# Kernel tuning notes

Measured on AMD Instinct MI355X. Metric: run time of the kernel, lower is better.

The kernel has to match this reference:

```python
import jax, jax.numpy as jnp
import numpy as np

EMBED_DIM = 768
NUM_HEADS = 12
HEAD_DIM = EMBED_DIM // NUM_HEADS


def setup_inputs() -> dict:
    key = jax.random.key(0)
    ks = jax.random.split(key, 9)
    B, S, D = 2, 2048, EMBED_DIM
    scale = 1.0 / np.sqrt(D)
    x = jax.random.normal(ks[0], (B, S, D), dtype=jnp.float32)
    Wq = jax.random.normal(ks[1], (D, D), dtype=jnp.float32) * scale
    bq = jax.random.normal(ks[2], (D,), dtype=jnp.float32) * 0.01
    Wk = jax.random.normal(ks[3], (D, D), dtype=jnp.float32) * scale
    bk = jax.random.normal(ks[4], (D,), dtype=jnp.float32) * 0.01
    Wv = jax.random.normal(ks[5], (D, D), dtype=jnp.float32) * scale
    bv = jax.random.normal(ks[6], (D,), dtype=jnp.float32) * 0.01
    Wo = jax.random.normal(ks[7], (D, D), dtype=jnp.float32) * scale
    bo = jax.random.normal(ks[8], (D,), dtype=jnp.float32) * 0.01
    return {"x": x, "Wq": Wq, "bq": bq, "Wk": Wk, "bk": bk,
            "Wv": Wv, "bv": bv, "Wo": Wo, "bo": bo}


def reference(x, Wq, bq, Wk, bk, Wv, bv, Wo, bo):
    B, S, D = x.shape
    H, Dh = NUM_HEADS, HEAD_DIM
    # separate QKV projections (weights stored [in, out] so y = x @ W + b)
    q = (x @ Wq + bq).reshape(B, S, H, Dh)
    k = (x @ Wk + bk).reshape(B, S, H, Dh)
    v = (x @ Wv + bv).reshape(B, S, H, Dh)
    # NOTE: original module applies NO 1/sqrt(head_dim) scaling
    scores = jnp.einsum('bqhd,bkhd->bhqk', q, k)          # [B,H,S,S] materialized
    attn = jax.nn.softmax(scores, axis=-1)
    ctx = jnp.einsum('bhqk,bkhd->bqhd', attn, v)          # [B,S,H,Dh]
    out = ctx.reshape(B, S, D) @ Wo + bo
    return out
```

## Files before the change

kernel.cpp:

```cpp
#include <hip/hip_runtime.h>
#include <hip/hip_bf16.h>


typedef __attribute__((ext_vector_type(8))) short short8;
typedef __attribute__((ext_vector_type(4))) float float4e;

__device__ __forceinline__ ushort f2bf(float f) {
    union { float f; unsigned u; } v; v.f = f;
    unsigned r = v.u + 0x7FFF + ((v.u >> 16) & 1);
    return (ushort)(r >> 16);
}

__global__ __launch_bounds__(256) void cast_f32_bf16(
    const float* __restrict__ in, ushort* __restrict__ out, int n4)
{
    int i = blockIdx.x * blockDim.x + threadIdx.x;
    if (i < n4) {
        float4 v = *(const float4*)&in[(size_t)i * 4];
        ushort4 o;
        o.x = f2bf(v.x); o.y = f2bf(v.y); o.z = f2bf(v.z); o.w = f2bf(v.w);
        *(ushort4*)&out[(size_t)i * 4] = o;
    }
}

__global__ __launch_bounds__(256) void transpose_cast_w(
    const float* __restrict__ W, ushort* __restrict__ Wt)
{
    __shared__ float t[64][65];
    const int tid = threadIdx.x;
    const int c  = tid & 63;
    const int rg = tid >> 6;
    const int k0 = blockIdx.y * 64, n0 = blockIdx.x * 64;
    #pragma unroll
    for (int r = 0; r < 16; ++r) {
        const int row = rg * 16 + r;
        t[row][c] = W[(size_t)(k0 + row) * 768 + n0 + c];
    }
    __syncthreads();
    #pragma unroll
    for (int r = 0; r < 16; ++r) {
        const int row = rg * 16 + r;
        Wt[(size_t)(n0 + row) * 768 + k0 + c] = f2bf(t[c][row]);
    }
}

__global__ __launch_bounds__(256) void transpose_v(
    const ushort* __restrict__ Vb, ushort* __restrict__ VT)
{
    __shared__ ushort t[64][72];
    const int tid = threadIdx.x;
    const int b = blockIdx.z, h = blockIdx.y, s0 = blockIdx.x * 64;
    const int lr = tid >> 3;
    const int lc = (tid & 7) * 8;

    #pragma unroll
    for (int half = 0; half < 64; half += 32) {
        const int row = lr + half;
        *(uint4*)&t[row][lc] =
            *(const uint4*)&Vb[(size_t)(b * 2048 + s0 + row) * 768 + h * 64 + lc];
    }
    __syncthreads();
    #pragma unroll
    for (int half = 0; half < 64; half += 32) {
        const int d = lr + half;
        ushort tmp[8];
        #pragma unroll
        for (int i = 0; i < 8; ++i) tmp[i] = t[lc + i][d];
        *(uint4*)&VT[((size_t)(b * 12 + h) * 64 + d) * 2048 + s0 + lc] =
            *(const uint4*)tmp;
    }
}

__global__ __launch_bounds__(256) void gemm_qkv_fused(
    const ushort* __restrict__ A, const ushort* __restrict__ Bt,
    const float* __restrict__ bq, const float* __restrict__ bk,
    const float* __restrict__ bv, ushort* __restrict__ Outbase)
{
    constexpr int K = 768;
    __shared__ ushort As[128][40];
    __shared__ ushort Bs[128][40];

    const int tid  = threadIdx.x;
    const int w    = tid >> 6;
    const int lane = tid & 63;
    const int l16  = lane & 15;
    const int quad = lane >> 4;
    const int wr   = (w >> 1) * 64;
    const int wc   = (w & 1) * 64;
    const int row0 = blockIdx.y * 128, col0 = blockIdx.x * 128;
    const int sr = tid >> 2, sc = (tid & 3) * 8;

    float4e acc[4][4];
    #pragma unroll
    for (int mi = 0; mi < 4; ++mi)
        #pragma unroll
        for (int ni = 0; ni < 4; ++ni) acc[mi][ni] = (float4e){0.f,0.f,0.f,0.f};

    uint4 a0 = *(const uint4*)&A [(size_t)(row0 + sr     ) * K + sc];
    uint4 a1 = *(const uint4*)&A [(size_t)(row0 + sr + 64) * K + sc];
    uint4 b0 = *(const uint4*)&Bt[(size_t)(col0 + sr     ) * K + sc];
    uint4 b1 = *(const uint4*)&Bt[(size_t)(col0 + sr + 64) * K + sc];

    for (int k0 = 0; k0 < K; k0 += 32) {
        *(uint4*)&As[sr     ][sc] = a0;
        *(uint4*)&As[sr + 64][sc] = a1;
        *(uint4*)&Bs[sr     ][sc] = b0;
        *(uint4*)&Bs[sr + 64][sc] = b1;
        __syncthreads();

        if (k0 + 32 < K) {
            const int kn = k0 + 32;
            a0 = *(const uint4*)&A [(size_t)(row0 + sr     ) * K + kn + sc];
            a1 = *(const uint4*)&A [(size_t)(row0 + sr + 64) * K + kn + sc];
            b0 = *(const uint4*)&Bt[(size_t)(col0 + sr     ) * K + kn + sc];
            b1 = *(const uint4*)&Bt[(size_t)(col0 + sr + 64) * K + kn + sc];
        }

        short8 af[4], bf[4];
        #pragma unroll
        for (int i = 0; i < 4; ++i) {
            af[i] = *(const short8*)&As[wr + i * 16 + l16][quad * 8];
            bf[i] = *(const short8*)&Bs[wc + i * 16 + l16][quad * 8];
        }
        #pragma unroll
        for (int mi = 0; mi < 4; ++mi)
            #pragma unroll
            for (int ni = 0; ni < 4; ++ni)
                acc[mi][ni] = __builtin_amdgcn_mfma_f32_16x16x32_bf16(
                    af[mi], bf[ni], acc[mi][ni], 0, 0, 0);
        __syncthreads();
    }

    const int seg = (col0 >= 1536) ? 2 : (col0 >= 768 ? 1 : 0);
    const float* bias = (seg == 0) ? bq : (seg == 1) ? bk : bv;
    const int ncol0 = col0 - seg * 768 + wc;
    ushort* outp = Outbase + (size_t)seg * (4096u * 768u);

    #pragma unroll
    for (int ni = 0; ni < 4; ++ni) {
        const int col = ncol0 + ni * 16 + l16;
        const float bs = bias[col];
        #pragma unroll
        for (int mi = 0; mi < 4; ++mi) {
            #pragma unroll
            for (int r = 0; r < 4; ++r) {
                const int row = row0 + wr + mi * 16 + quad * 4 + r;
                outp[(size_t)row * 768 + col] = f2bf(acc[mi][ni][r] + bs);
            }
        }
    }
}

__global__ __launch_bounds__(256) void gemm_bt_bias_f32(
    const ushort* __restrict__ A, const ushort* __restrict__ Bt,
    const float* __restrict__ bias, float* __restrict__ Cout,
    int M, int N, int K)
{
    __shared__ ushort As[64][40];
    __shared__ ushort Bs[64][40];

    const int tid  = threadIdx.x;
    const int w    = tid >> 6;
    const int lane = tid & 63;
    const int l16  = lane & 15;
    const int quad = lane >> 4;
    const int row0 = blockIdx.y * 64, col0 = blockIdx.x * 64;
    const int sr = tid >> 2, sc = (tid & 3) * 8;

    float4e acc[4];
    #pragma unroll
    for (int n = 0; n < 4; ++n) acc[n] = (float4e){0.f, 0.f, 0.f, 0.f};

    for (int k0 = 0; k0 < K; k0 += 32) {
        *(uint4*)&As[sr][sc] = *(const uint4*)&A [(size_t)(row0 + sr) * K + k0 + sc];
        *(uint4*)&Bs[sr][sc] = *(const uint4*)&Bt[(size_t)(col0 + sr) * K + k0 + sc];
        __syncthreads();

        const short8 a = *(const short8*)&As[w * 16 + l16][quad * 8];
        #pragma unroll
        for (int n = 0; n < 4; ++n) {
            const short8 b = *(const short8*)&Bs[n * 16 + l16][quad * 8];
            acc[n] = __builtin_amdgcn_mfma_f32_16x16x32_bf16(a, b, acc[n], 0, 0, 0);
        }
        __syncthreads();
    }

    #pragma unroll
    for (int n = 0; n < 4; ++n) {
        const int col = col0 + n * 16 + l16;
        const float bs = bias[col];
        #pragma unroll
        for (int r = 0; r < 4; ++r) {
            const int row = row0 + w * 16 + quad * 4 + r;
            Cout[(size_t)row * N + col] = acc[n][r] + bs;
        }
    }
}

__global__ __launch_bounds__(256) void attn_mfma(
    const ushort* __restrict__ Qg, const ushort* __restrict__ Kgl,
    const ushort* __restrict__ VT, ushort* __restrict__ Ctx)
{
    constexpr int S = 2048, D = 768;
    __shared__ ushort Ks [64][72];
    __shared__ ushort Vts[64][72];
    __shared__ ushort Ps [64][72];

    const int tid  = threadIdx.x;
    const int w    = tid >> 6;
    const int lane = tid & 63;
    const int l16  = lane & 15;
    const int quad = lane >> 4;
    const int b = blockIdx.z, h = blockIdx.y, q0 = blockIdx.x * 64;
    const size_t hc = (size_t)h * 64;

    const size_t qoff = (size_t)(b * S + q0 + w * 16 + l16) * D + hc + quad * 8;
    const short8 yq0 = *(const short8*)&Qg[qoff];
    const short8 yq1 = *(const short8*)&Qg[qoff + 32];

    float m_ = -1e30f, l_ = 0.f;
    float4e oa[4];
    #pragma unroll
    for (int n = 0; n < 4; ++n) oa[n] = (float4e){0.f, 0.f, 0.f, 0.f};

    const int sr = tid >> 2;
    const int sc = (tid & 3) * 16;
    const size_t vtb = ((size_t)(b * 12 + h) * 64 + sr) * 2048;

    uint4 kA, kB, vA, vB;
    {
        const size_t gk = (size_t)(b * S + sr) * D + hc + sc;
        kA = *(const uint4*)&Kgl[gk];
        kB = *(const uint4*)&Kgl[gk + 8];
        vA = *(const uint4*)&VT[vtb + sc];
        vB = *(const uint4*)&VT[vtb + sc + 8];
    }

    for (int k0 = 0; k0 < S; k0 += 64) {
        *(uint4*)&Ks [sr][sc    ] = kA;
        *(uint4*)&Ks [sr][sc + 8] = kB;
        *(uint4*)&Vts[sr][sc    ] = vA;
        *(uint4*)&Vts[sr][sc + 8] = vB;
        __syncthreads();

        if (k0 + 64 < S) {
            const size_t gk = (size_t)(b * S + k0 + 64 + sr) * D + hc + sc;
            kA = *(const uint4*)&Kgl[gk];
            kB = *(const uint4*)&Kgl[gk + 8];
            vA = *(const uint4*)&VT[vtb + k0 + 64 + sc];
            vB = *(const uint4*)&VT[vtb + k0 + 64 + sc + 8];
        }

        float4e sa[4];
        #pragma unroll
        for (int kb = 0; kb < 4; ++kb) {
            const short8 xk0 = *(const short8*)&Ks[kb * 16 + l16][quad * 8];
            const short8 xk1 = *(const short8*)&Ks[kb * 16 + l16][32 + quad * 8];
            float4e z = (float4e){0.f, 0.f, 0.f, 0.f};
            z      = __builtin_amdgcn_mfma_f32_16x16x32_bf16(xk0, yq0, z, 0, 0, 0);
            sa[kb] = __builtin_amdgcn_mfma_f32_16x16x32_bf16(xk1, yq1, z, 0, 0, 0);
        }

        float mx = -1e30f;
        #pragma unroll
        for (int kb = 0; kb < 4; ++kb)
            #pragma unroll
            for (int r = 0; r < 4; ++r) mx = fmaxf(mx, sa[kb][r]);
        mx = fmaxf(mx, __shfl_xor(mx, 16, 64));
        mx = fmaxf(mx, __shfl_xor(mx, 32, 64));
        const float mn = fmaxf(m_, mx);
        const float alpha = __expf(m_ - mn);
        float p[4][4], ps = 0.f;
        #pragma unroll
        for (int kb = 0; kb < 4; ++kb)
            #pragma unroll
            for (int r = 0; r < 4; ++r) {
                p[kb][r] = __expf(sa[kb][r] - mn);
                ps += p[kb][r];
            }
        ps += __shfl_xor(ps, 16, 64);
        ps += __shfl_xor(ps, 32, 64);
        l_ = l_ * alpha + ps;
        m_ = mn;

        #pragma unroll
        for (int kb = 0; kb < 4; ++kb) {
            ushort4 pk;
            pk.x = f2bf(p[kb][0]); pk.y = f2bf(p[kb][1]);
            pk.z = f2bf(p[kb][2]); pk.w = f2bf(p[kb][3]);
            *(ushort4*)&Ps[w * 16 + l16][kb * 16 + quad * 4] = pk;
        }

        #pragma unroll
        for (int n = 0; n < 4; ++n)
            #pragma unroll
            for (int r = 0; r < 4; ++r) oa[n][r] *= alpha;

        const short8 yp0 = *(const short8*)&Ps[w * 16 + l16][quad * 8];
        const short8 yp1 = *(const short8*)&Ps[w * 16 + l16][32 + quad * 8];
        #pragma unroll
        for (int db = 0; db < 4; ++db) {
            const short8 xv0 = *(const short8*)&Vts[db * 16 + l16][quad * 8];
            const short8 xv1 = *(const short8*)&Vts[db * 16 + l16][32 + quad * 8];
            oa[db] = __builtin_amdgcn_mfma_f32_16x16x32_bf16(xv0, yp0, oa[db], 0, 0, 0);
            oa[db] = __builtin_amdgcn_mfma_f32_16x16x32_bf16(xv1, yp1, oa[db], 0, 0, 0);
        }
        __syncthreads();
    }

    const float inv = 1.0f / l_;
    const size_t crow = (size_t)(b * S + q0 + w * 16 + l16) * D + hc;
    #pragma unroll
    for (int db = 0; db < 4; ++db) {
        ushort4 ov;
        ov.x = f2bf(oa[db][0] * inv); ov.y = f2bf(oa[db][1] * inv);
        ov.z = f2bf(oa[db][2] * inv); ov.w = f2bf(oa[db][3] * inv);
        *(ushort4*)&Ctx[crow + db * 16 + quad * 4] = ov;
    }
}

extern "C" void kernel_launch(void* const* d_in, const int* in_sizes, int n_in,
                              void* d_out, int out_size, void* d_ws, size_t ws_size,
                              hipStream_t stream)
{
    const float* x  = (const float*)d_in[0];
    const float* Wq = (const float*)d_in[1];
    const float* bq = (const float*)d_in[2];
    const float* Wk = (const float*)d_in[3];
    const float* bk = (const float*)d_in[4];
    const float* Wv = (const float*)d_in[5];
    const float* bv = (const float*)d_in[6];
    const float* Wo = (const float*)d_in[7];
    const float* bo = (const float*)d_in[8];

    const int M = 4096, D = 768;
    const size_t XE = (size_t)M * D;
    const size_t WE = (size_t)D * D;

    ushort* xb   = (ushort*)d_ws;
    ushort* wtq  = xb   + XE;
    ushort* wtk  = wtq  + WE;
    ushort* wtv  = wtk  + WE;
    ushort* wto  = wtv  + WE;
    ushort* qb   = wto  + WE;
    ushort* kb   = qb   + XE;
    ushort* vb   = kb   + XE;
    ushort* ctxb = vb   + XE;
    ushort* vt   = xb;

    cast_f32_bf16<<<(int)(XE / 4 / 256), 256, 0, stream>>>(x, xb, (int)(XE / 4));

    const dim3 gt(12, 12);
    transpose_cast_w<<<gt, 256, 0, stream>>>(Wq, wtq);
    transpose_cast_w<<<gt, 256, 0, stream>>>(Wk, wtk);
    transpose_cast_w<<<gt, 256, 0, stream>>>(Wv, wtv);
    transpose_cast_w<<<gt, 256, 0, stream>>>(Wo, wto);

    gemm_qkv_fused<<<dim3(2304 / 128, 4096 / 128), 256, 0, stream>>>(
        xb, wtq, bq, bk, bv, qb);

    transpose_v<<<dim3(32, 12, 2), 256, 0, stream>>>(vb, vt);

    attn_mfma<<<dim3(2048 / 64, 12, 2), 256, 0, stream>>>(qb, kb, vt, ctxb);

    gemm_bt_bias_f32<<<dim3(D / 64, M / 64), 256, 0, stream>>>(
        ctxb, wto, bo, (float*)d_out, M, D, D);
}
```

Baseline: 209.8 us.

## Enlarge attention KV tile, use 128x128 output GEMM, batch weight transposes

```diff
diff --git a/kernel.cpp b/kernel.cpp
--- a/kernel.cpp
+++ b/kernel.cpp
@@ -23,10 +23,16 @@
     }
 }
 
-__global__ __launch_bounds__(256) void transpose_cast_w(
-    const float* __restrict__ W, ushort* __restrict__ Wt)
+__global__ __launch_bounds__(256) void transpose_cast_w4(
+    const float* __restrict__ W0, const float* __restrict__ W1,
+    const float* __restrict__ W2, const float* __restrict__ W3,
+    ushort* __restrict__ WtBase)
 {
     __shared__ float t[64][65];
+    const int z = blockIdx.z;
+    const float* W = (z == 0) ? W0 : (z == 1) ? W1 : (z == 2) ? W2 : W3;
+    ushort* Wt = WtBase + (size_t)z * (768u * 768u);
+
     const int tid = threadIdx.x;
     const int c  = tid & 63;
     const int rg = tid >> 6;
@@ -151,48 +157,76 @@
     }
 }
 
-__global__ __launch_bounds__(256) void gemm_bt_bias_f32(
+__global__ __launch_bounds__(256) void gemm_wo_128(
     const ushort* __restrict__ A, const ushort* __restrict__ Bt,
-    const float* __restrict__ bias, float* __restrict__ Cout,
-    int M, int N, int K)
-{
-    __shared__ ushort As[64][40];
-    __shared__ ushort Bs[64][40];
+    const float* __restrict__ bias, float* __restrict__ Cout)
+{
+    constexpr int K = 768, N = 768;
+    __shared__ ushort As[128][40];
+    __shared__ ushort Bs[128][40];
 
     const int tid  = threadIdx.x;
     const int w    = tid >> 6;
     const int lane = tid & 63;
     const int l16  = lane & 15;
     const int quad = lane >> 4;
-    const int row0 = blockIdx.y * 64, col0 = blockIdx.x * 64;
+    const int wr   = (w >> 1) * 64;
+    const int wc   = (w & 1) * 64;
+    const int row0 = blockIdx.y * 128, col0 = blockIdx.x * 128;
     const int sr = tid >> 2, sc = (tid & 3) * 8;
 
-    float4e acc[4];
-    #pragma unroll
-    for (int n = 0; n < 4; ++n) acc[n] = (float4e){0.f, 0.f, 0.f, 0.f};
+    float4e acc[4][4];
+    #pragma unroll
+    for (int mi = 0; mi < 4; ++mi)
+        #pragma unroll
+        for (int ni = 0; ni < 4; ++ni) acc[mi][ni] = (float4e){0.f,0.f,0.f,0.f};
+
+    uint4 a0 = *(const uint4*)&A [(size_t)(row0 + sr     ) * K + sc];
+    uint4 a1 = *(const uint4*)&A [(size_t)(row0 + sr + 64) * K + sc];
+    uint4 b0 = *(const uint4*)&Bt[(size_t)(col0 + sr     ) * K + sc];
+    uint4 b1 = *(const uint4*)&Bt[(size_t)(col0 + sr + 64) * K + sc];
 
     for (int k0 = 0; k0 < K; k0 += 32) {
-        *(uint4*)&As[sr][sc] = *(const uint4*)&A [(size_t)(row0 + sr) * K + k0 + sc];
-        *(uint4*)&Bs[sr][sc] = *(const uint4*)&Bt[(size_t)(col0 + sr) * K + k0 + sc];
-        __syncthreads();
-
-        const short8 a = *(const short8*)&As[w * 16 + l16][quad * 8];
-        #pragma unroll
-        for (int n = 0; n < 4; ++n) {
-            const short8 b = *(const short8*)&Bs[n * 16 + l16][quad * 8];
-            acc[n] = __builtin_amdgcn_mfma_f32_16x16x32_bf16(a, b, acc[n], 0, 0, 0);
-        }
-        __syncthreads();
-    }
-
-    #pragma unroll
-    for (int n = 0; n < 4; ++n) {
-        const int col = col0 + n * 16 + l16;
+        *(uint4*)&As[sr     ][sc] = a0;
+        *(uint4*)&As[sr + 64][sc] = a1;
+        *(uint4*)&Bs[sr     ][sc] = b0;
+        *(uint4*)&Bs[sr + 64][sc] = b1;
+        __syncthreads();
+
+        if (k0 + 32 < K) {
+            const int kn = k0 + 32;
+            a0 = *(const uint4*)&A [(size_t)(row0 + sr     ) * K + kn + sc];
+            a1 = *(const uint4*)&A [(size_t)(row0 + sr + 64) * K + kn + sc];
+            b0 = *(const uint4*)&Bt[(size_t)(col0 + sr     ) * K + kn + sc];
+            b1 = *(const uint4*)&Bt[(size_t)(col0 + sr + 64) * K + kn + sc];
+        }
+
+        short8 af[4], bf[4];
+        #pragma unroll
+        for (int i = 0; i < 4; ++i) {
+            af[i] = *(const short8*)&As[wr + i * 16 + l16][quad * 8];
+            bf[i] = *(const short8*)&Bs[wc + i * 16 + l16][quad * 8];
+        }
+        #pragma unroll
+        for (int mi = 0; mi < 4; ++mi)
+            #pragma unroll
+            for (int ni = 0; ni < 4; ++ni)
+                acc[mi][ni] = __builtin_amdgcn_mfma_f32_16x16x32_bf16(
+                    af[mi], bf[ni], acc[mi][ni], 0, 0, 0);
+        __syncthreads();
+    }
+
+    #pragma unroll
+    for (int ni = 0; ni < 4; ++ni) {
+        const int col = col0 + wc + ni * 16 + l16;
         const float bs = bias[col];
         #pragma unroll
-        for (int r = 0; r < 4; ++r) {
-            const int row = row0 + w * 16 + quad * 4 + r;
-            Cout[(size_t)row * N + col] = acc[n][r] + bs;
+        for (int mi = 0; mi < 4; ++mi) {
+            #pragma unroll
+            for (int r = 0; r < 4; ++r) {
+                const int row = row0 + wr + mi * 16 + quad * 4 + r;
+                Cout[(size_t)row * N + col] = acc[mi][ni][r] + bs;
+            }
         }
     }
 }
@@ -201,10 +235,10 @@
     const ushort* __restrict__ Qg, const ushort* __restrict__ Kgl,
     const ushort* __restrict__ VT, ushort* __restrict__ Ctx)
 {
-    constexpr int S = 2048, D = 768;
-    __shared__ ushort Ks [64][72];
-    __shared__ ushort Vts[64][72];
-    __shared__ ushort Ps [64][72];
+    constexpr int S = 2048, D = 768, TK = 128;
+    __shared__ ushort Ks [128][68];
+    __shared__ ushort Vts[64][136];
+    __shared__ ushort Ps [64][136];
 
     const int tid  = threadIdx.x;
     const int w    = tid >> 6;
@@ -223,37 +257,36 @@
     #pragma unroll
     for (int n = 0; n < 4; ++n) oa[n] = (float4e){0.f, 0.f, 0.f, 0.f};
 
-    const int sr = tid >> 2;
-    const int sc = (tid & 3) * 16;
-    const size_t vtb = ((size_t)(b * 12 + h) * 64 + sr) * 2048;
-
-    uint4 kA, kB, vA, vB;
-    {
-        const size_t gk = (size_t)(b * S + sr) * D + hc + sc;
-        kA = *(const uint4*)&Kgl[gk];
-        kB = *(const uint4*)&Kgl[gk + 8];
-        vA = *(const uint4*)&VT[vtb + sc];
-        vB = *(const uint4*)&VT[vtb + sc + 8];
-    }
-
-    for (int k0 = 0; k0 < S; k0 += 64) {
-        *(uint4*)&Ks [sr][sc    ] = kA;
-        *(uint4*)&Ks [sr][sc + 8] = kB;
-        *(uint4*)&Vts[sr][sc    ] = vA;
-        *(uint4*)&Vts[sr][sc + 8] = vB;
-        __syncthreads();
-
-        if (k0 + 64 < S) {
-            const size_t gk = (size_t)(b * S + k0 + 64 + sr) * D + hc + sc;
-            kA = *(const uint4*)&Kgl[gk];
-            kB = *(const uint4*)&Kgl[gk + 8];
-            vA = *(const uint4*)&VT[vtb + k0 + 64 + sc];
-            vB = *(const uint4*)&VT[vtb + k0 + 64 + sc + 8];
-        }
-
-        float4e sa[4];
-        #pragma unroll
-        for (int kb = 0; kb < 4; ++kb) {
+    const int kr = tid >> 1, kc = (tid & 1) * 32;
+    const int dr = tid >> 2, vc = (tid & 3) * 32;
+    const size_t vtb = ((size_t)(b * 12 + h) * 64 + dr) * 2048;
+
+    uint4 kf[4], vf[4];
+    #pragma unroll
+    for (int j = 0; j < 4; ++j) {
+        kf[j] = *(const uint4*)&Kgl[(size_t)(b * S + kr) * D + hc + kc + 8 * j];
+        vf[j] = *(const uint4*)&VT[vtb + vc + 8 * j];
+    }
+
+    for (int k0 = 0; k0 < S; k0 += TK) {
+        #pragma unroll
+        for (int j = 0; j < 4; ++j) {
+            *(uint4*)&Ks [kr][kc + 8 * j] = kf[j];
+            *(uint4*)&Vts[dr][vc + 8 * j] = vf[j];
+        }
+        __syncthreads();
+
+        if (k0 + TK < S) {
+            #pragma unroll
+            for (int j = 0; j < 4; ++j) {
+                kf[j] = *(const uint4*)&Kgl[(size_t)(b * S + k0 + TK + kr) * D + hc + kc + 8 * j];
+                vf[j] = *(const uint4*)&VT[vtb + k0 + TK + vc + 8 * j];
+            }
+        }
+
+        float4e sa[8];
+        #pragma unroll
+        for (int kb = 0; kb < 8; ++kb) {
             const short8 xk0 = *(const short8*)&Ks[kb * 16 + l16][quad * 8];
             const short8 xk1 = *(const short8*)&Ks[kb * 16 + l16][32 + quad * 8];
             float4e z = (float4e){0.f, 0.f, 0.f, 0.f};
@@ -263,47 +296,43 @@
 
         float mx = -1e30f;
         #pragma unroll
-        for (int kb = 0; kb < 4; ++kb)
+        for (int kb = 0; kb < 8; ++kb)
             #pragma unroll
             for (int r = 0; r < 4; ++r) mx = fmaxf(mx, sa[kb][r]);
         mx = fmaxf(mx, __shfl_xor(mx, 16, 64));
         mx = fmaxf(mx, __shfl_xor(mx, 32, 64));
         const float mn = fmaxf(m_, mx);
         const float alpha = __expf(m_ - mn);
-        float p[4][4], ps = 0.f;
-        #pragma unroll
-        for (int kb = 0; kb < 4; ++kb)
-            #pragma unroll
-            for (int r = 0; r < 4; ++r) {
-                p[kb][r] = __expf(sa[kb][r] - mn);
-                ps += p[kb][r];
-            }
+        float ps = 0.f;
+        #pragma unroll
+        for (int kb = 0; kb < 8; ++kb) {
+            float p0 = __expf(sa[kb][0] - mn);
+            float p1 = __expf(sa[kb][1] - mn);
+            float p2 = __expf(sa[kb][2] - mn);
+            float p3 = __expf(sa[kb][3] - mn);
+            ps += (p0 + p1) + (p2 + p3);
+            ushort4 pk;
+            pk.x = f2bf(p0); pk.y = f2bf(p1); pk.z = f2bf(p2); pk.w = f2bf(p3);
+            *(ushort4*)&Ps[w * 16 + l16][kb * 16 + quad * 4] = pk;
+        }
         ps += __shfl_xor(ps, 16, 64);
         ps += __shfl_xor(ps, 32, 64);
         l_ = l_ * alpha + ps;
         m_ = mn;
 
         #pragma unroll
-        for (int kb = 0; kb < 4; ++kb) {
-            ushort4 pk;
-            pk.x = f2bf(p[kb][0]); pk.y = f2bf(p[kb][1]);
-            pk.z = f2bf(p[kb][2]); pk.w = f2bf(p[kb][3]);
-            *(ushort4*)&Ps[w * 16 + l16][kb * 16 + quad * 4] = pk;
-        }
-
-        #pragma unroll
         for (int n = 0; n < 4; ++n)
             #pragma unroll
             for (int r = 0; r < 4; ++r) oa[n][r] *= alpha;
 
-        const short8 yp0 = *(const short8*)&Ps[w * 16 + l16][quad * 8];
-        const short8 yp1 = *(const short8*)&Ps[w * 16 + l16][32 + quad * 8];
-        #pragma unroll
-        for (int db = 0; db < 4; ++db) {
-            const short8 xv0 = *(const short8*)&Vts[db * 16 + l16][quad * 8];
-            const short8 xv1 = *(const short8*)&Vts[db * 16 + l16][32 + quad * 8];
-            oa[db] = __builtin_amdgcn_mfma_f32_16x16x32_bf16(xv0, yp0, oa[db], 0, 0, 0);
-            oa[db] = __builtin_amdgcn_mfma_f32_16x16x32_bf16(xv1, yp1, oa[db], 0, 0, 0);
+        #pragma unroll
+        for (int c = 0; c < 4; ++c) {
+            const short8 yp = *(const short8*)&Ps[w * 16 + l16][c * 32 + quad * 8];
+            #pragma unroll
+            for (int db = 0; db < 4; ++db) {
+                const short8 xv = *(const short8*)&Vts[db * 16 + l16][c * 32 + quad * 8];
+                oa[db] = __builtin_amdgcn_mfma_f32_16x16x32_bf16(xv, yp, oa[db], 0, 0, 0);
+            }
         }
         __syncthreads();
     }
@@ -339,9 +368,7 @@
 
     ushort* xb   = (ushort*)d_ws;
     ushort* wtq  = xb   + XE;
-    ushort* wtk  = wtq  + WE;
-    ushort* wtv  = wtk  + WE;
-    ushort* wto  = wtv  + WE;
+    ushort* wto  = wtq  + 3 * WE;
     ushort* qb   = wto  + WE;
     ushort* kb   = qb   + XE;
     ushort* vb   = kb   + XE;
@@ -350,11 +377,7 @@
 
     cast_f32_bf16<<<(int)(XE / 4 / 256), 256, 0, stream>>>(x, xb, (int)(XE / 4));
 
-    const dim3 gt(12, 12);
-    transpose_cast_w<<<gt, 256, 0, stream>>>(Wq, wtq);
-    transpose_cast_w<<<gt, 256, 0, stream>>>(Wk, wtk);
-    transpose_cast_w<<<gt, 256, 0, stream>>>(Wv, wtv);
-    transpose_cast_w<<<gt, 256, 0, stream>>>(Wo, wto);
+    transpose_cast_w4<<<dim3(12, 12, 4), 256, 0, stream>>>(Wq, Wk, Wv, Wo, wtq);
 
     gemm_qkv_fused<<<dim3(2304 / 128, 4096 / 128), 256, 0, stream>>>(
         xb, wtq, bq, bk, bv, qb);
@@ -363,6 +386,6 @@
 
     attn_mfma<<<dim3(2048 / 64, 12, 2), 256, 0, stream>>>(qb, kb, vt, ctxb);
 
-    gemm_bt_bias_f32<<<dim3(D / 64, M / 64), 256, 0, stream>>>(
-        ctxb, wto, bo, (float*)d_out, M, D, D);
-}
+    gemm_wo_128<<<dim3(768 / 128, 4096 / 128), 256, 0, stream>>>(
+        ctxb, wto, bo, (float*)d_out);
+}
```

Result: slower. 277.8 us (+32.4%).

## Use async global-to-LDS loads in QKV GEMM, 128-tile Wo GEMM, batched weight transpose

Applied to the files above, without the earlier changes.

```diff
diff --git a/kernel.cpp b/kernel.cpp
--- a/kernel.cpp
+++ b/kernel.cpp
@@ -9,6 +9,13 @@
     union { float f; unsigned u; } v; v.f = f;
     unsigned r = v.u + 0x7FFF + ((v.u >> 16) & 1);
     return (ushort)(r >> 16);
+}
+
+__device__ __forceinline__ void async_cp16(const ushort* g, ushort* l) {
+    __builtin_amdgcn_global_load_lds(
+        (const __attribute__((address_space(1))) unsigned int*)g,
+        (__attribute__((address_space(3))) unsigned int*)l,
+        16, 0, 0);
 }
 
 __global__ __launch_bounds__(256) void cast_f32_bf16(
@@ -23,10 +30,16 @@
     }
 }
 
-__global__ __launch_bounds__(256) void transpose_cast_w(
-    const float* __restrict__ W, ushort* __restrict__ Wt)
+__global__ __launch_bounds__(256) void transpose_cast_w4(
+    const float* __restrict__ W0, const float* __restrict__ W1,
+    const float* __restrict__ W2, const float* __restrict__ W3,
+    ushort* __restrict__ WtBase)
 {
     __shared__ float t[64][65];
+    const int z = blockIdx.z;
+    const float* W = (z == 0) ? W0 : (z == 1) ? W1 : (z == 2) ? W2 : W3;
+    ushort* Wt = WtBase + (size_t)z * (768u * 768u);
+
     const int tid = threadIdx.x;
     const int c  = tid & 63;
     const int rg = tid >> 6;
@@ -77,6 +90,76 @@
     const float* __restrict__ bv, ushort* __restrict__ Outbase)
 {
     constexpr int K = 768;
+    __shared__ ushort As[128][32];
+    __shared__ ushort Bs[128][32];
+
+    const int tid  = threadIdx.x;
+    const int w    = tid >> 6;
+    const int lane = tid & 63;
+    const int l16  = lane & 15;
+    const int quad = lane >> 4;
+    const int wr   = (w >> 1) * 64;
+    const int wc   = (w & 1) * 64;
+    const int row0 = blockIdx.y * 128, col0 = blockIdx.x * 128;
+
+    const int r4 = lane >> 2;
+    const int c8 = (lane & 3) * 8;
+
+    float4e acc[4][4];
+    #pragma unroll
+    for (int mi = 0; mi < 4; ++mi)
+        #pragma unroll
+        for (int ni = 0; ni < 4; ++ni) acc[mi][ni] = (float4e){0.f,0.f,0.f,0.f};
+
+    for (int k0 = 0; k0 < K; k0 += 32) {
+        #pragma unroll
+        for (int i = 0; i < 2; ++i) {
+            const int rr = w * 32 + i * 16;
+            async_cp16(&A [(size_t)(row0 + rr + r4) * K + k0 + c8], &As[rr][0]);
+            async_cp16(&Bt[(size_t)(col0 + rr + r4) * K + k0 + c8], &Bs[rr][0]);
+        }
+        __syncthreads();
+
+        short8 af[4], bf[4];
+        #pragma unroll
+        for (int i = 0; i < 4; ++i) {
+            af[i] = *(const short8*)&As[wr + i * 16 + l16][quad * 8];
+            bf[i] = *(const short8*)&Bs[wc + i * 16 + l16][quad * 8];
+        }
+        #pragma unroll
+        for (int mi = 0; mi < 4; ++mi)
+            #pragma unroll
+            for (int ni = 0; ni < 4; ++ni)
+                acc[mi][ni] = __builtin_amdgcn_mfma_f32_16x16x32_bf16(
+                    af[mi], bf[ni], acc[mi][ni], 0, 0, 0);
+        __syncthreads();
+    }
+
+    const int seg = (col0 >= 1536) ? 2 : (col0 >= 768 ? 1 : 0);
+    const float* bias = (seg == 0) ? bq : (seg == 1) ? bk : bv;
+    const int ncol0 = col0 - seg * 768 + wc;
+    ushort* outp = Outbase + (size_t)seg * (4096u * 768u);
+
+    #pragma unroll
+    for (int ni = 0; ni < 4; ++ni) {
+        const int col = ncol0 + ni * 16 + l16;
+        const float bs = bias[col];
+        #pragma unroll
+        for (int mi = 0; mi < 4; ++mi) {
+            #pragma unroll
+            for (int r = 0; r < 4; ++r) {
+                const int row = row0 + wr + mi * 16 + quad * 4 + r;
+                outp[(size_t)row * 768 + col] = f2bf(acc[mi][ni][r] + bs);
+            }
+        }
+    }
+}
+
+__global__ __launch_bounds__(256) void gemm_wo_128(
+    const ushort* __restrict__ A, const ushort* __restrict__ Bt,
+    const float* __restrict__ bias, float* __restrict__ Cout)
+{
+    constexpr int K = 768, N = 768;
     __shared__ ushort As[128][40];
     __shared__ ushort Bs[128][40];
 
@@ -131,68 +214,17 @@
         __syncthreads();
     }
 
-    const int seg = (col0 >= 1536) ? 2 : (col0 >= 768 ? 1 : 0);
-    const float* bias = (seg == 0) ? bq : (seg == 1) ? bk : bv;
-    const int ncol0 = col0 - seg * 768 + wc;
-    ushort* outp = Outbase + (size_t)seg * (4096u * 768u);
-
     #pragma unroll
     for (int ni = 0; ni < 4; ++ni) {
-        const int col = ncol0 + ni * 16 + l16;
+        const int col = col0 + wc + ni * 16 + l16;
         const float bs = bias[col];
         #pragma unroll
         for (int mi = 0; mi < 4; ++mi) {
             #pragma unroll
             for (int r = 0; r < 4; ++r) {
                 const int row = row0 + wr + mi * 16 + quad * 4 + r;
-                outp[(size_t)row * 768 + col] = f2bf(acc[mi][ni][r] + bs);
+                Cout[(size_t)row * N + col] = acc[mi][ni][r] + bs;
             }
-        }
-    }
-}
-
-__global__ __launch_bounds__(256) void gemm_bt_bias_f32(
-    const ushort* __restrict__ A, const ushort* __restrict__ Bt,
-    const float* __restrict__ bias, float* __restrict__ Cout,
-    int M, int N, int K)
-{
-    __shared__ ushort As[64][40];
-    __shared__ ushort Bs[64][40];
-
-    const int tid  = threadIdx.x;
-    const int w    = tid >> 6;
-    const int lane = tid & 63;
-    const int l16  = lane & 15;
-    const int quad = lane >> 4;
-    const int row0 = blockIdx.y * 64, col0 = blockIdx.x * 64;
-    const int sr = tid >> 2, sc = (tid & 3) * 8;
-
-    float4e acc[4];
-    #pragma unroll
-    for (int n = 0; n < 4; ++n) acc[n] = (float4e){0.f, 0.f, 0.f, 0.f};
-
-    for (int k0 = 0; k0 < K; k0 += 32) {
-        *(uint4*)&As[sr][sc] = *(const uint4*)&A [(size_t)(row0 + sr) * K + k0 + sc];
-        *(uint4*)&Bs[sr][sc] = *(const uint4*)&Bt[(size_t)(col0 + sr) * K + k0 + sc];
-        __syncthreads();
-
-        const short8 a = *(const short8*)&As[w * 16 + l16][quad * 8];
-        #pragma unroll
-        for (int n = 0; n < 4; ++n) {
-            const short8 b = *(const short8*)&Bs[n * 16 + l16][quad * 8];
-            acc[n] = __builtin_amdgcn_mfma_f32_16x16x32_bf16(a, b, acc[n], 0, 0, 0);
-        }
-        __syncthreads();
-    }
-
-    #pragma unroll
-    for (int n = 0; n < 4; ++n) {
-        const int col = col0 + n * 16 + l16;
-        const float bs = bias[col];
-        #pragma unroll
-        for (int r = 0; r < 4; ++r) {
-            const int row = row0 + w * 16 + quad * 4 + r;
-            Cout[(size_t)row * N + col] = acc[n][r] + bs;
         }
     }
 }
@@ -339,9 +371,7 @@
 
     ushort* xb   = (ushort*)d_ws;
     ushort* wtq  = xb   + XE;
-    ushort* wtk  = wtq  + WE;
-    ushort* wtv  = wtk  + WE;
-    ushort* wto  = wtv  + WE;
+    ushort* wto  = wtq  + 3 * WE;
     ushort* qb   = wto  + WE;
     ushort* kb   = qb   + XE;
     ushort* vb   = kb   + XE;
@@ -350,11 +380,7 @@
 
     cast_f32_bf16<<<(int)(XE / 4 / 256), 256, 0, stream>>>(x, xb, (int)(XE / 4));
 
-    const dim3 gt(12, 12);
-    transpose_cast_w<<<gt, 256, 0, stream>>>(Wq, wtq);
-    transpose_cast_w<<<gt, 256, 0, stream>>>(Wk, wtk);
-    transpose_cast_w<<<gt, 256, 0, stream>>>(Wv, wtv);
-    transpose_cast_w<<<gt, 256, 0, stream>>>(Wo, wto);
+    transpose_cast_w4<<<dim3(12, 12, 4), 256, 0, stream>>>(Wq, Wk, Wv, Wo, wtq);
 
     gemm_qkv_fused<<<dim3(2304 / 128, 4096 / 128), 256, 0, stream>>>(
         xb, wtq, bq, bk, bv, qb);
@@ -363,6 +389,6 @@
 
     attn_mfma<<<dim3(2048 / 64, 12, 2), 256, 0, stream>>>(qb, kb, vt, ctxb);
 
-    gemm_bt_bias_f32<<<dim3(D / 64, M / 64), 256, 0, stream>>>(
-        ctxb, wto, bo, (float*)d_out, M, D, D);
-}
+    gemm_wo_128<<<dim3(768 / 128, 4096 / 128), 256, 0, stream>>>(
+        ctxb, wto, bo, (float*)d_out);
+}
```

New measurement: 194.7 us. 1.08x faster.
